# Performance work log

Measured on AMD Instinct MI355X. Metric: run time of the kernel, lower is better.

Reference implementation:

```python
import jax, jax.numpy as jnp
import numpy as np

# Dimensions: D must equal C_CHUNK**2 (original code's view+transpose requires it)
D = 4096        # flattened input dim per sample
C_CHUNK = 64    # chunk_size (rows of G per chunk)
N_CHUNKS = D // C_CHUNK  # = 64
H = 512         # hidden dim of forward_func MLP
C_OUT = 8       # output classes of forward_func
B = 8           # batch size (state_batch has 2*B rows)
EPS_G = 1e-4    # metric regularizer (constant under grad)


def setup_inputs() -> dict:
    key = jax.random.key(0)
    ks = jax.random.split(key, 6)
    t = jax.random.uniform(ks[0], (1,), dtype=jnp.float32)
    state_batch = jax.random.normal(ks[1], (2 * B, D), dtype=jnp.float32)
    x0_batch = jax.random.normal(ks[2], (B, D), dtype=jnp.float32)
    x1_batch = jax.random.normal(ks[3], (B, D), dtype=jnp.float32)
    W1 = jax.random.normal(ks[4], (D, H), dtype=jnp.float32) / np.float32(np.sqrt(D))
    W2 = jax.random.normal(ks[5], (H, C_OUT), dtype=jnp.float32) / np.float32(np.sqrt(H))
    return {"t": t, "state_batch": state_batch, "x0_batch": x0_batch,
            "x1_batch": x1_batch, "W1": W1, "W2": W2}


def _accel_per_sample(x, v, W1, W2):
    """Chunked Christoffel-symbol contraction for one sample.
    x: [D] current point, v: [D] deviation velocity. Returns a: [D]."""
    def f(xi):  # forward_func: 2-layer tanh MLP, [D] -> [C_OUT]
        return jnp.tanh(xi @ W1) @ W2

    ones = jnp.ones((D,), x.dtype)

    def chunk_sums(xi):
        # G = J^T J + eps*I; row_sums[i] = sum_j G[i,j] computed without
        # materializing the D x D metric: J^T (J @ 1)  (+ const eps on diag).
        J = jax.jacrev(f)(xi)              # [C_OUT, D]
        row = J.T @ (J @ ones)             # [D]
        return row.reshape(N_CHUNKS, C_CHUNK).sum(axis=1)  # [N_CHUNKS]

    g = jax.jacrev(chunk_sums)(x)          # [N_CHUNKS, D] = dG_chunk_sum/dx
    g = g.reshape(N_CHUNKS, C_CHUNK, C_CHUNK)
    g = g / (jnp.linalg.norm(g, axis=2, keepdims=True) + 1e-6)
    Gamma = 0.5 * (g + jnp.swapaxes(g, 1, 2))   # symmetrized [nc, c, c]
    vc = v.reshape(N_CHUNKS, C_CHUNK)
    # a_chunk[i] = -sum_k Gamma[i,k] v_i v_k  (Christoffel quadratic in v)
    a = -jnp.einsum('nik,ni,nk->ni', Gamma, vc, vc)
    return a.reshape(D)


def reference(t, state_batch, x0_batch, x1_batch, W1, W2):
    ts = t[0]
    Bn = state_batch.shape[0] // 2
    deviation = state_batch[:Bn]
    dev_velocity = state_batch[Bn:]
    window = 4.0 * ts * (1.0 - ts)
    x = x0_batch + ts * (x1_batch - x0_batch) + window * deviation  # [B, D]
    a = jax.vmap(_accel_per_sample, in_axes=(0, 0, None, None))(x, dev_velocity, W1, W2)
    a = a / (jnp.linalg.norm(dev_velocity, axis=1, keepdims=True) + 1e-6)
    restoration = -0.1 * deviation
    return jnp.concatenate([dev_velocity, a + restoration], axis=0)  # [2B, D]
```

## Files before the change

kernel.cpp:

```cpp
#include <hip/hip_runtime.h>

#define D 4096
#define H 512
#define NCH 64
#define CCH 64
#define B 8
#define COUT 8

#define OFF_P     0
#define OFF_UPART (OFF_P + NCH*H)
#define OFF_S     (OFF_UPART + NCH*B*H)
#define OFF_ST2   (OFF_S + B*H)
#define OFF_Q     (OFF_ST2 + B*H)
#define OFF_C     (OFF_Q + B*H)
#define OFF_VN    (OFF_C + H)
#define OFF_W     (OFF_VN + 8)
#define OFF_A1    (OFF_W + B*NCH*H)
#define OFF_Z     (OFF_A1 + B*NCH*CCH)
#define WS_FLOATS (OFF_Z + B*NCH*CCH)

__global__ void k0_zero(float* __restrict__ ws) {
    int idx = blockIdx.x * 256 + threadIdx.x;
    ws[OFF_Z + idx] = 0.f;
}

__global__ void k1_reduce_w1(const float* __restrict__ W1,
                             const float* __restrict__ state,
                             const float* __restrict__ x0,
                             const float* __restrict__ x1,
                             const float* __restrict__ tptr,
                             float* __restrict__ ws) {
    int n   = blockIdx.x;
    int ht  = blockIdx.y;
    int tid = threadIdx.x;
    int h   = ht * 128 + tid;

    __shared__ float xs[B][64];
    float ts = tptr[0];
    float window = 4.f * ts * (1.f - ts);
    if (tid < 64) {
        int d = n * 64 + tid;
        for (int b = 0; b < B; ++b) {
            float a0 = x0[b * D + d];
            float a1v = x1[b * D + d];
            float dev = state[b * D + d];
            xs[b][tid] = a0 + ts * (a1v - a0) + window * dev;
        }
    }
    __syncthreads();

    float p = 0.f;
    float up[B];
#pragma unroll
    for (int b = 0; b < B; ++b) up[b] = 0.f;
    const float* wrow = W1 + (size_t)(n * 64) * H + h;
    for (int j = 0; j < 64; ++j) {
        float wv = wrow[(size_t)j * H];
        p += wv;
#pragma unroll
        for (int b = 0; b < B; ++b) up[b] += wv * xs[b][j];
    }
    ws[OFF_P + n * H + h] = p;
    for (int b = 0; b < B; ++b) ws[OFF_UPART + (n * B + b) * H + h] = up[b];
}

__global__ void k2_sample(const float* __restrict__ W2,
                          const float* __restrict__ state,
                          float* __restrict__ ws) {
    int b = blockIdx.x;
    int h = threadIdx.x;
    __shared__ float red[512 * 8];
    __shared__ float msh[8];

    float u = 0.f, c = 0.f;
    for (int n = 0; n < NCH; ++n) {
        u += ws[OFF_UPART + (n * B + b) * H + h];
        c += ws[OFF_P + n * H + h];
    }
    float tt  = tanhf(u);
    float s   = 1.f - tt * tt;
    float st2 = -2.f * tt * s;
    ws[OFF_S   + b * H + h] = s;
    ws[OFF_ST2 + b * H + h] = st2;
    ws[OFF_C   + h] = c;

    float w2r[8];
#pragma unroll
    for (int o = 0; o < 8; ++o) w2r[o] = W2[h * 8 + o];

    float cs = c * s;
#pragma unroll
    for (int o = 0; o < 8; ++o) red[h * 8 + o] = cs * w2r[o];
    __syncthreads();
    for (int stp = 256; stp > 0; stp >>= 1) {
        if (h < stp) {
#pragma unroll
            for (int o = 0; o < 8; ++o) red[h * 8 + o] += red[(h + stp) * 8 + o];
        }
        __syncthreads();
    }
    if (h < 8) msh[h] = red[h];
    __syncthreads();
    float q = 0.f;
#pragma unroll
    for (int o = 0; o < 8; ++o) q += w2r[o] * msh[o];
    ws[OFF_Q + b * H + h] = q;

    float sq = 0.f;
    const float* v = state + (size_t)(B + b) * D;
    for (int j = 0; j < D / H; ++j) { float vv = v[j * H + h]; sq += vv * vv; }
    __syncthreads();
    red[h] = sq;
    __syncthreads();
    for (int stp = 256; stp > 0; stp >>= 1) {
        if (h < stp) red[h] += red[h + stp];
        __syncthreads();
    }
    if (h == 0) ws[OFF_VN + b] = sqrtf(red[0]) + 1e-6f;
}

__global__ void k3_w(const float* __restrict__ W2,
                     float* __restrict__ ws) {
    int n = blockIdx.x;
    int b = blockIdx.y;
    int h = threadIdx.x;
    __shared__ float red[512 * 8];
    __shared__ float msh[8];

    float P = ws[OFF_P + n * H + h];
    float s = ws[OFF_S + b * H + h];
    float ps = P * s;
    float w2r[8];
#pragma unroll
    for (int o = 0; o < 8; ++o) w2r[o] = W2[h * 8 + o];
#pragma unroll
    for (int o = 0; o < 8; ++o) red[h * 8 + o] = ps * w2r[o];
    __syncthreads();
    for (int stp = 256; stp > 0; stp >>= 1) {
        if (h < stp) {
#pragma unroll
            for (int o = 0; o < 8; ++o) red[h * 8 + o] += red[(h + stp) * 8 + o];
        }
        __syncthreads();
    }
    if (h < 8) msh[h] = red[h];
    __syncthreads();
    float r = 0.f;
#pragma unroll
    for (int o = 0; o < 8; ++o) r += w2r[o] * msh[o];
    float wv = ws[OFF_ST2 + b * H + h] * (P * ws[OFF_Q + b * H + h] + ws[OFF_C + h] * r);
    ws[OFF_W + ((size_t)(b * NCH + n)) * H + h] = wv;
}

#define KT 32
__global__ __launch_bounds__(256) void k4_gemm(const float* __restrict__ W1,
                                               const float* __restrict__ state,
                                               float* __restrict__ ws) {
    int it  = blockIdx.x;
    int b   = blockIdx.y;
    int tid = threadIdx.x;
    int tx = tid & 15, ty = tid >> 4;

    __shared__ float Ws[KT][68];
    __shared__ float As[KT][68];
    __shared__ float g_s[64][65];
    __shared__ float vs[D];
    __shared__ float coef_s[64];

    const float* v = state + (size_t)(B + b) * D;
    for (int r = 0; r < 4; ++r) {
        int idx = tid + r * 256;
        ((float4*)vs)[idx] = ((const float4*)v)[idx];
    }

    float acc[4][4];
#pragma unroll
    for (int i = 0; i < 4; ++i)
#pragma unroll
        for (int j = 0; j < 4; ++j) acc[i][j] = 0.f;

    const float* wbase  = ws + OFF_W + (size_t)(b * NCH) * H;
    const float* w1base = W1 + (size_t)(it * 64) * H;

    int lrow = tid >> 3;
    int lcol = tid & 7;

    for (int kk = 0; kk < H / KT; ++kk) {
        int h0 = kk * KT;
#pragma unroll
        for (int rr = 0; rr < 2; ++rr) {
            int row = lrow + rr * 32;
            float4 wv = *(const float4*)&w1base[(size_t)row * H + h0 + lcol * 4];
            float4 av = *(const float4*)&wbase [(size_t)row * H + h0 + lcol * 4];
            Ws[lcol * 4 + 0][row] = wv.x; Ws[lcol * 4 + 1][row] = wv.y;
            Ws[lcol * 4 + 2][row] = wv.z; Ws[lcol * 4 + 3][row] = wv.w;
            As[lcol * 4 + 0][row] = av.x; As[lcol * 4 + 1][row] = av.y;
            As[lcol * 4 + 2][row] = av.z; As[lcol * 4 + 3][row] = av.w;
        }
        __syncthreads();
#pragma unroll
        for (int hh = 0; hh < KT; ++hh) {
            float4 af = *(const float4*)&As[hh][ty * 4];
            float4 bf = *(const float4*)&Ws[hh][tx * 4];
            acc[0][0] += af.x * bf.x; acc[0][1] += af.x * bf.y; acc[0][2] += af.x * bf.z; acc[0][3] += af.x * bf.w;
            acc[1][0] += af.y * bf.x; acc[1][1] += af.y * bf.y; acc[1][2] += af.y * bf.z; acc[1][3] += af.y * bf.w;
            acc[2][0] += af.z * bf.x; acc[2][1] += af.z * bf.y; acc[2][2] += af.z * bf.z; acc[2][3] += af.z * bf.w;
            acc[3][0] += af.w * bf.x; acc[3][1] += af.w * bf.y; acc[3][2] += af.w * bf.z; acc[3][3] += af.w * bf.w;
        }
        __syncthreads();
    }

#pragma unroll
    for (int i = 0; i < 4; ++i)
#pragma unroll
        for (int j = 0; j < 4; ++j)
            g_s[ty * 4 + i][tx * 4 + j] = acc[i][j];
    __syncthreads();

    if (tid < 64) {
        int n = tid;
        float ss = 0.f, y = 0.f;
        for (int k = 0; k < 64; ++k) {
            float gv = g_s[n][k];
            ss += gv * gv;
            y  += gv * vs[n * 64 + k];
        }
        float nrm = sqrtf(ss) + 1e-6f;
        coef_s[n] = vs[n * 64 + it] / nrm;
        ws[OFF_A1 + (size_t)(b * NCH + n) * CCH + it] = y / nrm;
    }
    __syncthreads();

    float* z = ws + OFF_Z + (size_t)(b * NCH) * CCH;
    for (int r = 0; r < 16; ++r) {
        int idx = tid + r * 256;
        int n = idx >> 6, k = idx & 63;
        atomicAdd(&z[n * 64 + k], g_s[n][k] * coef_s[n]);
    }
}

__global__ void k5_final(const float* __restrict__ state,
                         const float* __restrict__ ws,
                         float* __restrict__ out) {
    int idx = blockIdx.x * 256 + threadIdx.x;
    float vel = state[32768 + idx];
    out[idx] = vel;
    int b = idx >> 12;
    float a1 = ws[OFF_A1 + (size_t)b * 4096 + (idx & 4095)];
    float zv = ws[OFF_Z  + (size_t)b * 4096 + (idx & 4095)];
    float av = -0.5f * vel * (a1 + zv) / ws[OFF_VN + b];
    out[32768 + idx] = av - 0.1f * state[idx];
}

extern "C" void kernel_launch(void* const* d_in, const int* in_sizes, int n_in,
                              void* d_out, int out_size, void* d_ws, size_t ws_size,
                              hipStream_t stream) {
    const float* t   = (const float*)d_in[0];
    const float* st  = (const float*)d_in[1];
    const float* x0  = (const float*)d_in[2];
    const float* x1  = (const float*)d_in[3];
    const float* W1  = (const float*)d_in[4];
    const float* W2  = (const float*)d_in[5];
    float* out = (float*)d_out;
    float* ws  = (float*)d_ws;

    hipLaunchKernelGGL(k0_zero,      dim3(128),      dim3(256), 0, stream, ws);
    hipLaunchKernelGGL(k1_reduce_w1, dim3(64, 4),    dim3(128), 0, stream, W1, st, x0, x1, t, ws);
    hipLaunchKernelGGL(k2_sample,    dim3(8),        dim3(512), 0, stream, W2, st, ws);
    hipLaunchKernelGGL(k3_w,         dim3(64, 8),    dim3(512), 0, stream, W2, ws);
    hipLaunchKernelGGL(k4_gemm,      dim3(64, 8),    dim3(256), 0, stream, W1, st, ws);
    hipLaunchKernelGGL(k5_final,     dim3(128),      dim3(256), 0, stream, st, ws, out);
}
```

Measured before the change: 135.9 us.

## Use split-bf16 MFMA for chunk GEMM, shuffle reductions, drop atomics

The FP32 LDS-tiled GEMM in k4 becomes bf16 MFMA 16x16x32 with a hi/lo split (three MFMAs per tile) to keep near-fp32 accuracy. W1 and the W coefficients are split into bf16 pairs inside k1 and k3. k2 and k3 switch from shared-memory tree reductions to wave shuffles, and k3 runs one 64-thread wave per block. The atomicAdd accumulation into z becomes per-block partial buffers that k5 sums, so the zeroing kernel is removed. In exchange the workspace grows considerably (64 partial z slabs per sample plus the bf16 copies), and the result carries a small precision loss from the split bf16.

```diff
diff --git a/kernel.cpp b/kernel.cpp
--- a/kernel.cpp
+++ b/kernel.cpp
@@ -7,21 +7,30 @@
 #define B 8
 #define COUT 8
 
-#define OFF_P     0
-#define OFF_UPART (OFF_P + NCH*H)
-#define OFF_S     (OFF_UPART + NCH*B*H)
-#define OFF_ST2   (OFF_S + B*H)
-#define OFF_Q     (OFF_ST2 + B*H)
-#define OFF_C     (OFF_Q + B*H)
-#define OFF_VN    (OFF_C + H)
-#define OFF_W     (OFF_VN + 8)
-#define OFF_A1    (OFF_W + B*NCH*H)
-#define OFF_Z     (OFF_A1 + B*NCH*CCH)
-#define WS_FLOATS (OFF_Z + B*NCH*CCH)
-
-__global__ void k0_zero(float* __restrict__ ws) {
-    int idx = blockIdx.x * 256 + threadIdx.x;
-    ws[OFF_Z + idx] = 0.f;
+typedef __bf16 bf16x8 __attribute__((ext_vector_type(8)));
+typedef float  f32x4  __attribute__((ext_vector_type(4)));
+
+#define OFF_P    0
+#define OFF_UP   (OFF_P + NCH*H)
+#define OFF_S    (OFF_UP + NCH*B*H)
+#define OFF_ST2  (OFF_S + B*H)
+#define OFF_Q    (OFF_ST2 + B*H)
+#define OFF_C    (OFF_Q + B*H)
+#define OFF_VN   (OFF_C + H)
+#define OFF_A1   (OFF_VN + 64)
+#define OFF_ZB   (OFF_A1 + B*NCH*CCH)
+#define OFF_W1H  (OFF_ZB + B*64*4096)
+#define OFF_W1L  (OFF_W1H + (D*H)/2)
+#define OFF_WH   (OFF_W1L + (D*H)/2)
+#define OFF_WL   (OFF_WH + (B*NCH*H)/2)
+
+__device__ __forceinline__ unsigned short f2bf(float x) {
+    unsigned int u = __float_as_uint(x);
+    unsigned int r = (u + 0x7FFFu + ((u >> 16) & 1u)) >> 16;
+    return (unsigned short)r;
+}
+__device__ __forceinline__ float bf2f(unsigned short s) {
+    return __uint_as_float(((unsigned int)s) << 16);
 }
 
 __global__ void k1_reduce_w1(const float* __restrict__ W1,
@@ -49,32 +58,40 @@
     }
     __syncthreads();
 
+    unsigned short* __restrict__ W1Hp = (unsigned short*)(ws + OFF_W1H);
+    unsigned short* __restrict__ W1Lp = (unsigned short*)(ws + OFF_W1L);
+
     float p = 0.f;
     float up[B];
 #pragma unroll
     for (int b = 0; b < B; ++b) up[b] = 0.f;
-    const float* wrow = W1 + (size_t)(n * 64) * H + h;
     for (int j = 0; j < 64; ++j) {
-        float wv = wrow[(size_t)j * H];
+        int d = n * 64 + j;
+        float wv = W1[(size_t)d * H + h];
+        unsigned short hi = f2bf(wv);
+        W1Hp[d * H + h] = hi;
+        W1Lp[d * H + h] = f2bf(wv - bf2f(hi));
         p += wv;
 #pragma unroll
         for (int b = 0; b < B; ++b) up[b] += wv * xs[b][j];
     }
     ws[OFF_P + n * H + h] = p;
-    for (int b = 0; b < B; ++b) ws[OFF_UPART + (n * B + b) * H + h] = up[b];
+    for (int b = 0; b < B; ++b) ws[OFF_UP + (n * B + b) * H + h] = up[b];
 }
 
 __global__ void k2_sample(const float* __restrict__ W2,
                           const float* __restrict__ state,
                           float* __restrict__ ws) {
-    int b = blockIdx.x;
-    int h = threadIdx.x;
-    __shared__ float red[512 * 8];
-    __shared__ float msh[8];
-
+    int b = blockIdx.x, tid = threadIdx.x;
+    int wid = tid >> 6, lane = tid & 63;
+    __shared__ float lm[8][8];
+    __shared__ float ms[8];
+    __shared__ float lv[8];
+
+    int h = tid;
     float u = 0.f, c = 0.f;
     for (int n = 0; n < NCH; ++n) {
-        u += ws[OFF_UPART + (n * B + b) * H + h];
+        u += ws[OFF_UP + (n * B + b) * H + h];
         c += ws[OFF_P + n * H + h];
     }
     float tt  = tanhf(u);
@@ -84,158 +101,187 @@
     ws[OFF_ST2 + b * H + h] = st2;
     ws[OFF_C   + h] = c;
 
-    float w2r[8];
-#pragma unroll
-    for (int o = 0; o < 8; ++o) w2r[o] = W2[h * 8 + o];
+    const float4* w2p = (const float4*)(W2 + h * 8);
+    float4 w2a = w2p[0], w2b = w2p[1];
+    float w2r[8] = {w2a.x, w2a.y, w2a.z, w2a.w, w2b.x, w2b.y, w2b.z, w2b.w};
 
     float cs = c * s;
-#pragma unroll
-    for (int o = 0; o < 8; ++o) red[h * 8 + o] = cs * w2r[o];
-    __syncthreads();
-    for (int stp = 256; stp > 0; stp >>= 1) {
-        if (h < stp) {
-#pragma unroll
-            for (int o = 0; o < 8; ++o) red[h * 8 + o] += red[(h + stp) * 8 + o];
-        }
-        __syncthreads();
-    }
-    if (h < 8) msh[h] = red[h];
-    __syncthreads();
+    float pr[8];
+#pragma unroll
+    for (int o = 0; o < 8; ++o) pr[o] = cs * w2r[o];
+#pragma unroll
+    for (int mk = 1; mk < 64; mk <<= 1)
+#pragma unroll
+        for (int o = 0; o < 8; ++o) pr[o] += __shfl_xor(pr[o], mk);
+    if (lane == 0)
+#pragma unroll
+        for (int o = 0; o < 8; ++o) lm[wid][o] = pr[o];
+
+    float v2 = 0.f;
+    const float* v = state + (size_t)(B + b) * D;
+    for (int j = 0; j < D / H; ++j) { float vv = v[j * H + h]; v2 += vv * vv; }
+#pragma unroll
+    for (int mk = 1; mk < 64; mk <<= 1) v2 += __shfl_xor(v2, mk);
+    if (lane == 0) lv[wid] = v2;
+    __syncthreads();
+
+    if (tid < 8) {
+        float a = 0.f;
+        for (int w = 0; w < 8; ++w) a += lm[w][tid];
+        ms[tid] = a;
+    }
+    if (tid == 0) {
+        float a = 0.f;
+        for (int w = 0; w < 8; ++w) a += lv[w];
+        ws[OFF_VN + b] = sqrtf(a) + 1e-6f;
+    }
+    __syncthreads();
+
     float q = 0.f;
 #pragma unroll
-    for (int o = 0; o < 8; ++o) q += w2r[o] * msh[o];
+    for (int o = 0; o < 8; ++o) q += w2r[o] * ms[o];
     ws[OFF_Q + b * H + h] = q;
-
-    float sq = 0.f;
-    const float* v = state + (size_t)(B + b) * D;
-    for (int j = 0; j < D / H; ++j) { float vv = v[j * H + h]; sq += vv * vv; }
-    __syncthreads();
-    red[h] = sq;
-    __syncthreads();
-    for (int stp = 256; stp > 0; stp >>= 1) {
-        if (h < stp) red[h] += red[h + stp];
-        __syncthreads();
-    }
-    if (h == 0) ws[OFF_VN + b] = sqrtf(red[0]) + 1e-6f;
 }
 
 __global__ void k3_w(const float* __restrict__ W2,
                      float* __restrict__ ws) {
-    int n = blockIdx.x;
-    int b = blockIdx.y;
-    int h = threadIdx.x;
-    __shared__ float red[512 * 8];
-    __shared__ float msh[8];
-
-    float P = ws[OFF_P + n * H + h];
-    float s = ws[OFF_S + b * H + h];
-    float ps = P * s;
-    float w2r[8];
-#pragma unroll
-    for (int o = 0; o < 8; ++o) w2r[o] = W2[h * 8 + o];
-#pragma unroll
-    for (int o = 0; o < 8; ++o) red[h * 8 + o] = ps * w2r[o];
-    __syncthreads();
-    for (int stp = 256; stp > 0; stp >>= 1) {
-        if (h < stp) {
-#pragma unroll
-            for (int o = 0; o < 8; ++o) red[h * 8 + o] += red[(h + stp) * 8 + o];
-        }
-        __syncthreads();
-    }
-    if (h < 8) msh[h] = red[h];
-    __syncthreads();
-    float r = 0.f;
-#pragma unroll
-    for (int o = 0; o < 8; ++o) r += w2r[o] * msh[o];
-    float wv = ws[OFF_ST2 + b * H + h] * (P * ws[OFF_Q + b * H + h] + ws[OFF_C + h] * r);
-    ws[OFF_W + ((size_t)(b * NCH + n)) * H + h] = wv;
-}
-
-#define KT 32
-__global__ __launch_bounds__(256) void k4_gemm(const float* __restrict__ W1,
-                                               const float* __restrict__ state,
+    int n = blockIdx.x, b = blockIdx.y, lane = threadIdx.x;
+    float M[8];
+#pragma unroll
+    for (int o = 0; o < 8; ++o) M[o] = 0.f;
+    for (int j = 0; j < 8; ++j) {
+        int h = j * 64 + lane;
+        float ps = ws[OFF_P + n * H + h] * ws[OFF_S + b * H + h];
+        const float4* wp = (const float4*)(W2 + h * 8);
+        float4 wa = wp[0], wb = wp[1];
+        M[0] += ps * wa.x; M[1] += ps * wa.y; M[2] += ps * wa.z; M[3] += ps * wa.w;
+        M[4] += ps * wb.x; M[5] += ps * wb.y; M[6] += ps * wb.z; M[7] += ps * wb.w;
+    }
+#pragma unroll
+    for (int mk = 1; mk < 64; mk <<= 1)
+#pragma unroll
+        for (int o = 0; o < 8; ++o) M[o] += __shfl_xor(M[o], mk);
+
+    unsigned short* __restrict__ WHp = (unsigned short*)(ws + OFF_WH);
+    unsigned short* __restrict__ WLp = (unsigned short*)(ws + OFF_WL);
+    for (int j = 0; j < 8; ++j) {
+        int h = j * 64 + lane;
+        const float4* wp = (const float4*)(W2 + h * 8);
+        float4 wa = wp[0], wb = wp[1];
+        float r = wa.x*M[0] + wa.y*M[1] + wa.z*M[2] + wa.w*M[3]
+                + wb.x*M[4] + wb.y*M[5] + wb.z*M[6] + wb.w*M[7];
+        float P = ws[OFF_P + n * H + h];
+        float wv = ws[OFF_ST2 + b * H + h] * (P * ws[OFF_Q + b * H + h] + ws[OFF_C + h] * r);
+        unsigned short hi = f2bf(wv);
+        WHp[(b * NCH + n) * H + h] = hi;
+        WLp[(b * NCH + n) * H + h] = f2bf(wv - bf2f(hi));
+    }
+}
+
+__global__ __launch_bounds__(256) void k4_mfma(const float* __restrict__ state,
                                                float* __restrict__ ws) {
-    int it  = blockIdx.x;
+    int i   = blockIdx.x;
     int b   = blockIdx.y;
     int tid = threadIdx.x;
-    int tx = tid & 15, ty = tid >> 4;
-
-    __shared__ float Ws[KT][68];
-    __shared__ float As[KT][68];
-    __shared__ float g_s[64][65];
-    __shared__ float vs[D];
-    __shared__ float coef_s[64];
+    int wid = tid >> 6, lane = tid & 63;
+    int r16 = lane & 15;
+    int kgrp = (lane >> 4) * 8;
+
+    __shared__ float vsp[64][65];
+    __shared__ float gp[2][64][67];
+    __shared__ float coefs[64];
 
     const float* v = state + (size_t)(B + b) * D;
     for (int r = 0; r < 4; ++r) {
-        int idx = tid + r * 256;
-        ((float4*)vs)[idx] = ((const float4*)v)[idx];
-    }
-
-    float acc[4][4];
-#pragma unroll
-    for (int i = 0; i < 4; ++i)
-#pragma unroll
-        for (int j = 0; j < 4; ++j) acc[i][j] = 0.f;
-
-    const float* wbase  = ws + OFF_W + (size_t)(b * NCH) * H;
-    const float* w1base = W1 + (size_t)(it * 64) * H;
-
-    int lrow = tid >> 3;
-    int lcol = tid & 7;
-
-    for (int kk = 0; kk < H / KT; ++kk) {
-        int h0 = kk * KT;
-#pragma unroll
-        for (int rr = 0; rr < 2; ++rr) {
-            int row = lrow + rr * 32;
-            float4 wv = *(const float4*)&w1base[(size_t)row * H + h0 + lcol * 4];
-            float4 av = *(const float4*)&wbase [(size_t)row * H + h0 + lcol * 4];
-            Ws[lcol * 4 + 0][row] = wv.x; Ws[lcol * 4 + 1][row] = wv.y;
-            Ws[lcol * 4 + 2][row] = wv.z; Ws[lcol * 4 + 3][row] = wv.w;
-            As[lcol * 4 + 0][row] = av.x; As[lcol * 4 + 1][row] = av.y;
-            As[lcol * 4 + 2][row] = av.z; As[lcol * 4 + 3][row] = av.w;
+        int fidx = tid + r * 256;
+        float4 val = ((const float4*)v)[fidx];
+        int base = fidx * 4, row = base >> 6, col = base & 63;
+        vsp[row][col] = val.x; vsp[row][col+1] = val.y;
+        vsp[row][col+2] = val.z; vsp[row][col+3] = val.w;
+    }
+
+    const unsigned short* __restrict__ W1Hp = (const unsigned short*)(ws + OFF_W1H);
+    const unsigned short* __restrict__ W1Lp = (const unsigned short*)(ws + OFF_W1L);
+    const unsigned short* __restrict__ WHp  = (const unsigned short*)(ws + OFF_WH);
+    const unsigned short* __restrict__ WLp  = (const unsigned short*)(ws + OFF_WL);
+
+    f32x4 acc[4][4];
+    f32x4 z4 = {0.f, 0.f, 0.f, 0.f};
+#pragma unroll
+    for (int m = 0; m < 4; ++m)
+#pragma unroll
+        for (int c = 0; c < 4; ++c) acc[m][c] = z4;
+
+    int kb = wid * 128 + kgrp;
+#pragma unroll
+    for (int ks = 0; ks < 4; ++ks) {
+        int k = kb + ks * 32;
+        bf16x8 ah[4], al[4], bh[4], bl[4];
+#pragma unroll
+        for (int m = 0; m < 4; ++m) {
+            int off = (b * 64 + m * 16 + r16) * H + k;
+            ah[m] = *(const bf16x8*)(WHp + off);
+            al[m] = *(const bf16x8*)(WLp + off);
         }
-        __syncthreads();
-#pragma unroll
-        for (int hh = 0; hh < KT; ++hh) {
-            float4 af = *(const float4*)&As[hh][ty * 4];
-            float4 bf = *(const float4*)&Ws[hh][tx * 4];
-            acc[0][0] += af.x * bf.x; acc[0][1] += af.x * bf.y; acc[0][2] += af.x * bf.z; acc[0][3] += af.x * bf.w;
-            acc[1][0] += af.y * bf.x; acc[1][1] += af.y * bf.y; acc[1][2] += af.y * bf.z; acc[1][3] += af.y * bf.w;
-            acc[2][0] += af.z * bf.x; acc[2][1] += af.z * bf.y; acc[2][2] += af.z * bf.z; acc[2][3] += af.z * bf.w;
-            acc[3][0] += af.w * bf.x; acc[3][1] += af.w * bf.y; acc[3][2] += af.w * bf.z; acc[3][3] += af.w * bf.w;
+#pragma unroll
+        for (int c = 0; c < 4; ++c) {
+            int off = (i * 64 + c * 16 + r16) * H + k;
+            bh[c] = *(const bf16x8*)(W1Hp + off);
+            bl[c] = *(const bf16x8*)(W1Lp + off);
         }
-        __syncthreads();
-    }
-
-#pragma unroll
-    for (int i = 0; i < 4; ++i)
-#pragma unroll
-        for (int j = 0; j < 4; ++j)
-            g_s[ty * 4 + i][tx * 4 + j] = acc[i][j];
+#pragma unroll
+        for (int m = 0; m < 4; ++m)
+#pragma unroll
+            for (int c = 0; c < 4; ++c) {
+                acc[m][c] = __builtin_amdgcn_mfma_f32_16x16x32_bf16(ah[m], bh[c], acc[m][c], 0, 0, 0);
+                acc[m][c] = __builtin_amdgcn_mfma_f32_16x16x32_bf16(ah[m], bl[c], acc[m][c], 0, 0, 0);
+                acc[m][c] = __builtin_amdgcn_mfma_f32_16x16x32_bf16(al[m], bh[c], acc[m][c], 0, 0, 0);
+            }
+    }
+
+    int rowb = (lane >> 4) * 4;
+    if (wid < 2) {
+        float (*g)[67] = gp[wid];
+#pragma unroll
+        for (int m = 0; m < 4; ++m)
+#pragma unroll
+            for (int c = 0; c < 4; ++c)
+#pragma unroll
+                for (int e = 0; e < 4; ++e)
+                    g[m * 16 + rowb + e][c * 16 + r16] = acc[m][c][e];
+    }
+    __syncthreads();
+    if (wid >= 2) {
+        float (*g)[67] = gp[wid - 2];
+#pragma unroll
+        for (int m = 0; m < 4; ++m)
+#pragma unroll
+            for (int c = 0; c < 4; ++c)
+#pragma unroll
+                for (int e = 0; e < 4; ++e)
+                    g[m * 16 + rowb + e][c * 16 + r16] += acc[m][c][e];
+    }
     __syncthreads();
 
     if (tid < 64) {
         int n = tid;
         float ss = 0.f, y = 0.f;
         for (int k = 0; k < 64; ++k) {
-            float gv = g_s[n][k];
-            ss += gv * gv;
-            y  += gv * vs[n * 64 + k];
+            float g = gp[0][n][k] + gp[1][n][k];
+            ss += g * g;
+            y  += g * vsp[n][k];
         }
         float nrm = sqrtf(ss) + 1e-6f;
-        coef_s[n] = vs[n * 64 + it] / nrm;
-        ws[OFF_A1 + (size_t)(b * NCH + n) * CCH + it] = y / nrm;
-    }
-    __syncthreads();
-
-    float* z = ws + OFF_Z + (size_t)(b * NCH) * CCH;
+        ws[OFF_A1 + (size_t)(b * NCH + n) * CCH + i] = y / nrm;
+        coefs[n] = vsp[n][i] / nrm;
+    }
+    __syncthreads();
+
+    float* zb = ws + OFF_ZB + ((size_t)b * 64 + i) * 4096;
     for (int r = 0; r < 16; ++r) {
         int idx = tid + r * 256;
         int n = idx >> 6, k = idx & 63;
-        atomicAdd(&z[n * 64 + k], g_s[n][k] * coef_s[n]);
+        zb[idx] = (gp[0][n][k] + gp[1][n][k]) * coefs[n];
     }
 }
 
@@ -245,10 +291,12 @@
     int idx = blockIdx.x * 256 + threadIdx.x;
     float vel = state[32768 + idx];
     out[idx] = vel;
-    int b = idx >> 12;
-    float a1 = ws[OFF_A1 + (size_t)b * 4096 + (idx & 4095)];
-    float zv = ws[OFF_Z  + (size_t)b * 4096 + (idx & 4095)];
-    float av = -0.5f * vel * (a1 + zv) / ws[OFF_VN + b];
+    int b = idx >> 12, e = idx & 4095;
+    const float* zb = ws + OFF_ZB + (size_t)b * 64 * 4096 + e;
+    float z = 0.f;
+    for (int i = 0; i < 64; ++i) z += zb[(size_t)i * 4096];
+    float a1 = ws[OFF_A1 + (size_t)b * 4096 + e];
+    float av = -0.5f * vel * (a1 + z) / ws[OFF_VN + b];
     out[32768 + idx] = av - 0.1f * state[idx];
 }
 
@@ -264,10 +312,9 @@
     float* out = (float*)d_out;
     float* ws  = (float*)d_ws;
 
-    hipLaunchKernelGGL(k0_zero,      dim3(128),      dim3(256), 0, stream, ws);
-    hipLaunchKernelGGL(k1_reduce_w1, dim3(64, 4),    dim3(128), 0, stream, W1, st, x0, x1, t, ws);
-    hipLaunchKernelGGL(k2_sample,    dim3(8),        dim3(512), 0, stream, W2, st, ws);
-    hipLaunchKernelGGL(k3_w,         dim3(64, 8),    dim3(512), 0, stream, W2, ws);
-    hipLaunchKernelGGL(k4_gemm,      dim3(64, 8),    dim3(256), 0, stream, W1, st, ws);
-    hipLaunchKernelGGL(k5_final,     dim3(128),      dim3(256), 0, stream, st, ws, out);
-}
+    hipLaunchKernelGGL(k1_reduce_w1, dim3(64, 4), dim3(128), 0, stream, W1, st, x0, x1, t, ws);
+    hipLaunchKernelGGL(k2_sample,    dim3(8),     dim3(512), 0, stream, W2, st, ws);
+    hipLaunchKernelGGL(k3_w,         dim3(64, 8), dim3(64),  0, stream, W2, ws);
+    hipLaunchKernelGGL(k4_mfma,      dim3(64, 8), dim3(256), 0, stream, st, ws);
+    hipLaunchKernelGGL(k5_final,     dim3(128),   dim3(256), 0, stream, st, ws, out);
+}
```

Result: faster. 117.7 us (-13.4%).
